# Optimization experiments

Hardware: AMD Instinct MI355X
Metric: run time of the kernel (lower is better)

Reference implementation:

```python
import jax, jax.numpy as jnp
import numpy as np

B, T, IN, OUT, H = 1024, 25, 96, 96, 2048


def setup_inputs() -> dict:
    key = jax.random.key(0)
    ks = jax.random.split(key, 16)
    s = 0.05  # small init scale to keep gates in linear-ish region
    return {
        "input": jax.random.normal(ks[0], (B, IN), jnp.float32),
        "future_poses": jax.random.normal(ks[1], (B, T, OUT), jnp.float32),
        "hiddens": jax.random.normal(ks[2], (2, B, H), jnp.float32) * s,
        "W_ih0": jax.random.normal(ks[3], (3 * H, IN), jnp.float32) * s,
        "W_hh0": jax.random.normal(ks[4], (3 * H, H), jnp.float32) * s,
        "b_ih0": jax.random.normal(ks[5], (3 * H,), jnp.float32) * s,
        "b_hh0": jax.random.normal(ks[6], (3 * H,), jnp.float32) * s,
        "W_ih1": jax.random.normal(ks[7], (3 * H, H), jnp.float32) * s,
        "W_hh1": jax.random.normal(ks[8], (3 * H, H), jnp.float32) * s,
        "b_ih1": jax.random.normal(ks[9], (3 * H,), jnp.float32) * s,
        "b_hh1": jax.random.normal(ks[10], (3 * H,), jnp.float32) * s,
        "W_fc": jax.random.normal(ks[11], (OUT, H), jnp.float32) * s,
        "b_fc": jax.random.normal(ks[12], (OUT,), jnp.float32) * s,
        "teacher_forcing_rate": 0,
    }


def gru_cell(x, h, W_ih, W_hh, b_ih, b_hh):
    # PyTorch nn.GRUCell math; gate order [r, z, n]
    gi = x @ W_ih.T + b_ih
    gh = h @ W_hh.T + b_hh
    i_r, i_z, i_n = jnp.split(gi, 3, axis=-1)
    h_r, h_z, h_n = jnp.split(gh, 3, axis=-1)
    r = jax.nn.sigmoid(i_r + h_r)
    z = jax.nn.sigmoid(i_z + h_z)
    n = jnp.tanh(i_n + r * h_n)
    return (1.0 - z) * n + z * h


def reference(input, future_poses, hiddens, W_ih0, W_hh0, b_ih0, b_hh0,
              W_ih1, W_hh1, b_ih1, b_hh1, W_fc, b_fc, teacher_forcing_rate):
    # dropout p=0.0 (eval) -> identity; teacher_forcing_rate=0 -> always
    def step(carry, _):
        dec_in, h0, h1 = carry
        h0 = gru_cell(dec_in, h0, W_ih0, W_hh0, b_ih0, b_hh0)
        h1 = gru_cell(h0, h1, W_ih1, W_hh1, b_ih1, b_hh1)
        out = jax.nn.sigmoid(h1 @ W_fc.T + b_fc)  # [B, OUT]
        dec_in = jax.lax.stop_gradient(out)       # torch .detach()
        return (dec_in, h0, h1), out

    carry0 = (input, hiddens[0], hiddens[1])
    _, outs = jax.lax.scan(step, carry0, None, length=T)  # [T, B, OUT]
    return jnp.transpose(outs, (1, 0, 2))  # [B, T, OUT]
```

## Files before the change

kernel.cpp:

```cpp
#include <hip/hip_runtime.h>
#include <stdint.h>

typedef __bf16 bf16;
typedef __attribute__((ext_vector_type(8))) __bf16 bf16x8;
typedef __attribute__((ext_vector_type(4))) float f32x4;

#define GRU_H 2048
#define ODIM 96
#define PADX 128
#define BATCH 1024
#define TSTEPS 25

__device__ __forceinline__ float sigm(float x) { return 1.f / (1.f + __expf(-x)); }

__device__ __forceinline__ void gload16(const void* g, void* l) {
  __builtin_amdgcn_global_load_lds((const __attribute__((address_space(1))) uint32_t*)g,
                                   (__attribute__((address_space(3))) uint32_t*)l, 16, 0, 0);
}

__global__ void k_cvt(const float* __restrict__ s, bf16* __restrict__ d, int n) {
  int stride = gridDim.x * blockDim.x;
  for (int i = blockIdx.x * blockDim.x + threadIdx.x; i < n; i += stride)
    d[i] = (bf16)s[i];
}

__global__ void k_cvt_pad(const float* __restrict__ s, bf16* __restrict__ d,
                          int rows, int cin, int cout) {
  int n = rows * cout;
  int stride = gridDim.x * blockDim.x;
  for (int i = blockIdx.x * blockDim.x + threadIdx.x; i < n; i += stride) {
    int r = i / cout, c = i - r * cout;
    d[i] = (c < cin) ? (bf16)s[r * cin + c] : (bf16)0.f;
  }
}

__global__ void k_init_h(const float* __restrict__ s, float* __restrict__ hf,
                         bf16* __restrict__ hb, int n) {
  int stride = gridDim.x * blockDim.x;
  for (int i = blockIdx.x * blockDim.x + threadIdx.x; i < n; i += stride) {
    float v = s[i];
    hf[i] = v;
    hb[i] = (bf16)v;
  }
}

__global__ __launch_bounds__(512, 1) void k_gru(
    const bf16* __restrict__ xb, int kx,
    const bf16* __restrict__ hb,
    const bf16* __restrict__ wih,
    const bf16* __restrict__ whh,
    const float* __restrict__ bih, const float* __restrict__ bhh,
    const float* __restrict__ hprevf,
    float* __restrict__ hnewf, bf16* __restrict__ hnewb) {
  __shared__ alignas(16) char sm[3][40960];

  const int tid = threadIdx.x;
  const int l = tid & 63;
  const int w = tid >> 6;
  const int wm = w >> 1, wn = w & 1;
  const int bn0 = blockIdx.x * 64;
  const int bm0 = blockIdx.y * 128;
  const int lm = l >> 4, ln = l & 15;

  const int S1 = GRU_H / 64;
  const int S2 = kx / 64;
  const int S = S1 + S2;

  f32x4 accR[2][2] = {};
  f32x4 accZ[2][2] = {};
  f32x4 accNH[2][2] = {};
  f32x4 accNI[2][2] = {};

  auto stageStep = [&](int buf, int step) {
    const bf16* A; const bf16* W; int K; int k0;
    if (step < S1) { A = hb; W = whh; K = GRU_H; k0 = step * 64; }
    else           { A = xb; W = wih; K = kx;    k0 = (step - S1) * 64; }
    char* sb = &sm[buf][0];
#pragma unroll
    for (int it = 0; it < 2; ++it) {
      int c = it * 512 + tid;
      int row = c >> 3, pos = c & 7, slot = pos ^ (row & 7);
      const bf16* src = A + (size_t)(bm0 + row) * K + k0 + slot * 8;
      char* dst = sb + ((it * 512 + (tid & ~63)) << 4);
      gload16(src, dst);
    }
#pragma unroll
    for (int it = 0; it < 3; ++it) {
      int c = it * 512 + tid;
      int row = c >> 3, pos = c & 7, slot = pos ^ (row & 7);
      int g = row >> 6, r = row & 63;
      const bf16* src = W + (size_t)(g * GRU_H + bn0 + r) * K + k0 + slot * 8;
      char* dst = sb + 16384 + ((it * 512 + (tid & ~63)) << 4);
      gload16(src, dst);
    }
  };

  auto computeStep = [&](int buf, f32x4 (&accN)[2][2]) {
    const char* bp = &sm[buf][0];
#pragma unroll
    for (int kf = 0; kf < 2; ++kf) {
      bf16x8 af[2];
#pragma unroll
      for (int mf = 0; mf < 2; ++mf) {
        int row = wm * 32 + mf * 16 + ln;
        int pos = (kf * 4 + lm) ^ (row & 7);
        af[mf] = *(const bf16x8*)(bp + row * 128 + (pos << 4));
      }
      bf16x8 bq[3][2];
#pragma unroll
      for (int g = 0; g < 3; ++g)
#pragma unroll
        for (int nf = 0; nf < 2; ++nf) {
          int row = g * 64 + wn * 32 + nf * 16 + ln;
          int pos = (kf * 4 + lm) ^ (row & 7);
          bq[g][nf] = *(const bf16x8*)(bp + 16384 + row * 128 + (pos << 4));
        }
#pragma unroll
      for (int mf = 0; mf < 2; ++mf)
#pragma unroll
        for (int nf = 0; nf < 2; ++nf) {
          accR[mf][nf] = __builtin_amdgcn_mfma_f32_16x16x32_bf16(af[mf], bq[0][nf], accR[mf][nf], 0, 0, 0);
          accZ[mf][nf] = __builtin_amdgcn_mfma_f32_16x16x32_bf16(af[mf], bq[1][nf], accZ[mf][nf], 0, 0, 0);
          accN[mf][nf] = __builtin_amdgcn_mfma_f32_16x16x32_bf16(af[mf], bq[2][nf], accN[mf][nf], 0, 0, 0);
        }
    }
  };

  stageStep(0, 0);
  stageStep(1, 1);

  int bc = 0;
  for (int s = 0; s < S; ++s) {
    if (s + 2 < S) {
      int b2 = bc + 2; if (b2 >= 3) b2 -= 3;
      stageStep(b2, s + 2);
      asm volatile("s_waitcnt vmcnt(10)" ::: "memory");
    } else if (s + 1 < S) {
      asm volatile("s_waitcnt vmcnt(5)" ::: "memory");
    } else {
      asm volatile("s_waitcnt vmcnt(0)" ::: "memory");
    }
    __builtin_amdgcn_s_barrier();
    if (s < S1) computeStep(bc, accNH);
    else        computeStep(bc, accNI);
    asm volatile("s_waitcnt lgkmcnt(0)" ::: "memory");
    __builtin_amdgcn_s_barrier();
    ++bc; if (bc == 3) bc = 0;
  }

#pragma unroll
  for (int nf = 0; nf < 2; ++nf) {
    int j = bn0 + wn * 32 + nf * 16 + ln;
    float br = bih[j] + bhh[j];
    float bz = bih[GRU_H + j] + bhh[GRU_H + j];
    float bin = bih[2 * GRU_H + j];
    float bhn = bhh[2 * GRU_H + j];
#pragma unroll
    for (int mf = 0; mf < 2; ++mf) {
#pragma unroll
      for (int rr = 0; rr < 4; ++rr) {
        int m = bm0 + wm * 32 + mf * 16 + lm * 4 + rr;
        size_t idx = (size_t)m * GRU_H + j;
        float hp = hprevf[idx];
        float rg = sigm(accR[mf][nf][rr] + br);
        float zg = sigm(accZ[mf][nf][rr] + bz);
        float ng = tanhf(accNI[mf][nf][rr] + bin + rg * (accNH[mf][nf][rr] + bhn));
        float hn = (1.f - zg) * ng + zg * hp;
        hnewf[idx] = hn;
        hnewb[idx] = (bf16)hn;
      }
    }
  }
}

__global__ __launch_bounds__(256, 1) void k_fc_part(const bf16* __restrict__ h1b,
                                                    const bf16* __restrict__ wfc,
                                                    float* __restrict__ part) {
  const int kc = blockIdx.x;
  const int mt = blockIdx.y;
  const int l = threadIdx.x & 63, w = threadIdx.x >> 6;
  const int lm = l >> 4, ln = l & 15;
  const int m0 = mt * 64 + w * 16;
  const int k0 = kc * 128;
  f32x4 acc[6] = {};
#pragma unroll
  for (int kf = 0; kf < 4; ++kf) {
    bf16x8 a = *(const bf16x8*)&h1b[(size_t)(m0 + ln) * GRU_H + k0 + kf * 32 + lm * 8];
#pragma unroll
    for (int nf = 0; nf < 6; ++nf) {
      bf16x8 b = *(const bf16x8*)&wfc[(size_t)(nf * 16 + ln) * GRU_H + k0 + kf * 32 + lm * 8];
      acc[nf] = __builtin_amdgcn_mfma_f32_16x16x32_bf16(a, b, acc[nf], 0, 0, 0);
    }
  }
  float* base = part + (size_t)kc * (BATCH * ODIM);
#pragma unroll
  for (int nf = 0; nf < 6; ++nf)
#pragma unroll
    for (int rr = 0; rr < 4; ++rr)
      base[(size_t)(m0 + lm * 4 + rr) * ODIM + nf * 16 + ln] = acc[nf][rr];
}

__global__ void k_fc_red(const float* __restrict__ part, const float* __restrict__ bfc,
                         float* __restrict__ dout, bf16* __restrict__ decb, int t) {
  int i = blockIdx.x * blockDim.x + threadIdx.x;
  if (i >= BATCH * ODIM) return;
  int m = i / ODIM, n = i - m * ODIM;
  float s = bfc[n];
#pragma unroll
  for (int kc = 0; kc < 16; ++kc) s += part[(size_t)kc * (BATCH * ODIM) + i];
  s = sigm(s);
  dout[(size_t)m * (TSTEPS * ODIM) + t * ODIM + n] = s;
  decb[m * PADX + n] = (bf16)s;
}

extern "C" void kernel_launch(void* const* d_in, const int* in_sizes, int n_in,
                              void* d_out, int out_size, void* d_ws, size_t ws_size,
                              hipStream_t stream) {
  const float* input   = (const float*)d_in[0];
  const float* hiddens = (const float*)d_in[2];
  const float* W_ih0   = (const float*)d_in[3];
  const float* W_hh0   = (const float*)d_in[4];
  const float* b_ih0   = (const float*)d_in[5];
  const float* b_hh0   = (const float*)d_in[6];
  const float* W_ih1   = (const float*)d_in[7];
  const float* W_hh1   = (const float*)d_in[8];
  const float* b_ih1   = (const float*)d_in[9];
  const float* b_hh1   = (const float*)d_in[10];
  const float* W_fc    = (const float*)d_in[11];
  const float* b_fc    = (const float*)d_in[12];
  float* out = (float*)d_out;

  char* p = (char*)d_ws;
  auto take = [&](size_t n) { char* q = p; p += (n + 255) & ~(size_t)255; return q; };
  bf16* wih0b = (bf16*)take((size_t)3 * GRU_H * PADX * 2);
  bf16* whh0b = (bf16*)take((size_t)3 * GRU_H * GRU_H * 2);
  bf16* wih1b = (bf16*)take((size_t)3 * GRU_H * GRU_H * 2);
  bf16* whh1b = (bf16*)take((size_t)3 * GRU_H * GRU_H * 2);
  bf16* wfcb  = (bf16*)take((size_t)ODIM * GRU_H * 2);
  bf16* decb  = (bf16*)take((size_t)BATCH * PADX * 2);
  float* h0f[2], *h1f[2];
  bf16* h0b[2], *h1b[2];
  h0f[0] = (float*)take((size_t)BATCH * GRU_H * 4);
  h0f[1] = (float*)take((size_t)BATCH * GRU_H * 4);
  h1f[0] = (float*)take((size_t)BATCH * GRU_H * 4);
  h1f[1] = (float*)take((size_t)BATCH * GRU_H * 4);
  h0b[0] = (bf16*)take((size_t)BATCH * GRU_H * 2);
  h0b[1] = (bf16*)take((size_t)BATCH * GRU_H * 2);
  h1b[0] = (bf16*)take((size_t)BATCH * GRU_H * 2);
  h1b[1] = (bf16*)take((size_t)BATCH * GRU_H * 2);
  float* fcpart = (float*)take((size_t)16 * BATCH * ODIM * 4);

  k_cvt_pad<<<768, 256, 0, stream>>>(W_ih0, wih0b, 3 * GRU_H, ODIM, PADX);
  k_cvt<<<2048, 256, 0, stream>>>(W_hh0, whh0b, 3 * GRU_H * GRU_H);
  k_cvt<<<2048, 256, 0, stream>>>(W_ih1, wih1b, 3 * GRU_H * GRU_H);
  k_cvt<<<2048, 256, 0, stream>>>(W_hh1, whh1b, 3 * GRU_H * GRU_H);
  k_cvt<<<192, 256, 0, stream>>>(W_fc, wfcb, ODIM * GRU_H);
  k_cvt_pad<<<512, 256, 0, stream>>>(input, decb, BATCH, ODIM, PADX);
  k_init_h<<<2048, 256, 0, stream>>>(hiddens, h0f[0], h0b[0], BATCH * GRU_H);
  k_init_h<<<2048, 256, 0, stream>>>(hiddens + (size_t)BATCH * GRU_H, h1f[0], h1b[0], BATCH * GRU_H);

  int cur = 0;
  for (int t = 0; t < TSTEPS; ++t) {
    int nxt = cur ^ 1;
    k_gru<<<dim3(32, 8), 512, 0, stream>>>(decb, PADX, h0b[cur], wih0b, whh0b,
                                           b_ih0, b_hh0, h0f[cur], h0f[nxt], h0b[nxt]);
    k_gru<<<dim3(32, 8), 512, 0, stream>>>(h0b[nxt], GRU_H, h1b[cur], wih1b, whh1b,
                                           b_ih1, b_hh1, h1f[cur], h1f[nxt], h1b[nxt]);
    k_fc_part<<<dim3(16, 16), 256, 0, stream>>>(h1b[nxt], wfcb, fcpart);
    k_fc_red<<<384, 256, 0, stream>>>(fcpart, b_fc, out, decb, t);
    cur = nxt;
  }
}
```

Baseline: 2.830 ms.

## Shrink GRU GEMM tile to 64x64 with 256 threads and double buffering

The fused GRU gate GEMM kernel now uses 64-row M tiles with 4 waves of 256 threads, each wave owning a 16-column slice across all 64 rows, instead of 128-row tiles with 8 waves. The grid doubles to 512 blocks, and the 3-stage LDS ring with split barriers becomes a 2-buffer ping-pong using 64KB LDS. Dropping the launch-bound minimum of one block allows two or more blocks per CU, which should improve occupancy and latency hiding on 256 CUs. The cost is that each weight tile is reused across fewer batch rows, so weight traffic from L2 doubles. The pipeline is also shallower, with a full vmcnt(0) wait every step.

```diff
diff --git a/kernel.cpp b/kernel.cpp
--- a/kernel.cpp
+++ b/kernel.cpp
@@ -44,7 +44,7 @@
   }
 }
 
-__global__ __launch_bounds__(512, 1) void k_gru(
+__global__ __launch_bounds__(256) void k_gru(
     const bf16* __restrict__ xb, int kx,
     const bf16* __restrict__ hb,
     const bf16* __restrict__ wih,
@@ -52,119 +52,107 @@
     const float* __restrict__ bih, const float* __restrict__ bhh,
     const float* __restrict__ hprevf,
     float* __restrict__ hnewf, bf16* __restrict__ hnewb) {
-  __shared__ alignas(16) char sm[3][40960];
+  __shared__ alignas(16) char sm[2][32768];
 
   const int tid = threadIdx.x;
   const int l = tid & 63;
-  const int w = tid >> 6;
-  const int wm = w >> 1, wn = w & 1;
+  const int wn = tid >> 6;
+  const int wb = tid & ~63;
   const int bn0 = blockIdx.x * 64;
-  const int bm0 = blockIdx.y * 128;
+  const int bm0 = blockIdx.y * 64;
   const int lm = l >> 4, ln = l & 15;
+  char* sm0 = &sm[0][0];
 
   const int S1 = GRU_H / 64;
   const int S2 = kx / 64;
-  const int S = S1 + S2;
-
-  f32x4 accR[2][2] = {};
-  f32x4 accZ[2][2] = {};
-  f32x4 accNH[2][2] = {};
-  f32x4 accNI[2][2] = {};
-
-  auto stageStep = [&](int buf, int step) {
-    const bf16* A; const bf16* W; int K; int k0;
-    if (step < S1) { A = hb; W = whh; K = GRU_H; k0 = step * 64; }
-    else           { A = xb; W = wih; K = kx;    k0 = (step - S1) * 64; }
-    char* sb = &sm[buf][0];
+
+  f32x4 accR[4] = {};
+  f32x4 accZ[4] = {};
+  f32x4 accNH[4] = {};
+  f32x4 accNI[4] = {};
+
+  auto stage = [&](int lb2, const bf16* __restrict__ A, const bf16* __restrict__ W,
+                   int K, int k0) {
+    char* sb = sm0 + lb2;
 #pragma unroll
     for (int it = 0; it < 2; ++it) {
-      int c = it * 512 + tid;
+      int c = it * 256 + tid;
       int row = c >> 3, pos = c & 7, slot = pos ^ (row & 7);
-      const bf16* src = A + (size_t)(bm0 + row) * K + k0 + slot * 8;
-      char* dst = sb + ((it * 512 + (tid & ~63)) << 4);
-      gload16(src, dst);
-    }
-#pragma unroll
-    for (int it = 0; it < 3; ++it) {
-      int c = it * 512 + tid;
+      gload16(A + (size_t)(bm0 + row) * K + k0 + slot * 8,
+              sb + ((it * 256 + wb) << 4));
+    }
+#pragma unroll
+    for (int it = 0; it < 6; ++it) {
+      int c = it * 256 + tid;
       int row = c >> 3, pos = c & 7, slot = pos ^ (row & 7);
       int g = row >> 6, r = row & 63;
-      const bf16* src = W + (size_t)(g * GRU_H + bn0 + r) * K + k0 + slot * 8;
-      char* dst = sb + 16384 + ((it * 512 + (tid & ~63)) << 4);
-      gload16(src, dst);
+      gload16(W + (size_t)(g * GRU_H + bn0 + r) * K + k0 + slot * 8,
+              sb + 8192 + ((it * 256 + wb) << 4));
     }
   };
 
-  auto computeStep = [&](int buf, f32x4 (&accN)[2][2]) {
-    const char* bp = &sm[buf][0];
+  auto computeStep = [&](int lb2, f32x4 (&accN)[4]) {
+    const char* bp = sm0 + lb2;
 #pragma unroll
     for (int kf = 0; kf < 2; ++kf) {
-      bf16x8 af[2];
-#pragma unroll
-      for (int mf = 0; mf < 2; ++mf) {
-        int row = wm * 32 + mf * 16 + ln;
+      bf16x8 af[4];
+#pragma unroll
+      for (int mf = 0; mf < 4; ++mf) {
+        int row = mf * 16 + ln;
         int pos = (kf * 4 + lm) ^ (row & 7);
         af[mf] = *(const bf16x8*)(bp + row * 128 + (pos << 4));
       }
-      bf16x8 bq[3][2];
-#pragma unroll
-      for (int g = 0; g < 3; ++g)
-#pragma unroll
-        for (int nf = 0; nf < 2; ++nf) {
-          int row = g * 64 + wn * 32 + nf * 16 + ln;
-          int pos = (kf * 4 + lm) ^ (row & 7);
-          bq[g][nf] = *(const bf16x8*)(bp + 16384 + row * 128 + (pos << 4));
-        }
-#pragma unroll
-      for (int mf = 0; mf < 2; ++mf)
-#pragma unroll
-        for (int nf = 0; nf < 2; ++nf) {
-          accR[mf][nf] = __builtin_amdgcn_mfma_f32_16x16x32_bf16(af[mf], bq[0][nf], accR[mf][nf], 0, 0, 0);
-          accZ[mf][nf] = __builtin_amdgcn_mfma_f32_16x16x32_bf16(af[mf], bq[1][nf], accZ[mf][nf], 0, 0, 0);
-          accN[mf][nf] = __builtin_amdgcn_mfma_f32_16x16x32_bf16(af[mf], bq[2][nf], accN[mf][nf], 0, 0, 0);
-        }
+#pragma unroll
+      for (int g = 0; g < 3; ++g) {
+        int row = g * 64 + wn * 16 + ln;
+        int pos = (kf * 4 + lm) ^ (row & 7);
+        bf16x8 bq = *(const bf16x8*)(bp + 8192 + row * 128 + (pos << 4));
+        f32x4* accG = (g == 0) ? accR : (g == 1) ? accZ : accN;
+#pragma unroll
+        for (int mf = 0; mf < 4; ++mf)
+          accG[mf] = __builtin_amdgcn_mfma_f32_16x16x32_bf16(af[mf], bq, accG[mf], 0, 0, 0);
+      }
     }
   };
 
-  stageStep(0, 0);
-  stageStep(1, 1);
-
-  int bc = 0;
-  for (int s = 0; s < S; ++s) {
-    if (s + 2 < S) {
-      int b2 = bc + 2; if (b2 >= 3) b2 -= 3;
-      stageStep(b2, s + 2);
-      asm volatile("s_waitcnt vmcnt(10)" ::: "memory");
-    } else if (s + 1 < S) {
-      asm volatile("s_waitcnt vmcnt(5)" ::: "memory");
+  stage(0, hb, whh, GRU_H, 0);
+  asm volatile("s_waitcnt vmcnt(0)\ns_barrier" ::: "memory");
+
+  int lb = 0;
+  for (int s = 0; s < S1; ++s) {
+    if (s + 1 < S1) stage(lb ^ 32768, hb, whh, GRU_H, (s + 1) * 64);
+    else            stage(lb ^ 32768, xb, wih, kx, 0);
+    computeStep(lb, accNH);
+    asm volatile("s_waitcnt vmcnt(0) lgkmcnt(0)\ns_barrier" ::: "memory");
+    lb ^= 32768;
+  }
+  for (int s = 0; s < S2; ++s) {
+    if (s + 1 < S2) {
+      stage(lb ^ 32768, xb, wih, kx, (s + 1) * 64);
+      computeStep(lb, accNI);
+      asm volatile("s_waitcnt vmcnt(0) lgkmcnt(0)\ns_barrier" ::: "memory");
+      lb ^= 32768;
     } else {
-      asm volatile("s_waitcnt vmcnt(0)" ::: "memory");
-    }
-    __builtin_amdgcn_s_barrier();
-    if (s < S1) computeStep(bc, accNH);
-    else        computeStep(bc, accNI);
-    asm volatile("s_waitcnt lgkmcnt(0)" ::: "memory");
-    __builtin_amdgcn_s_barrier();
-    ++bc; if (bc == 3) bc = 0;
-  }
-
-#pragma unroll
-  for (int nf = 0; nf < 2; ++nf) {
-    int j = bn0 + wn * 32 + nf * 16 + ln;
+      computeStep(lb, accNI);
+    }
+  }
+
+  {
+    int j = bn0 + wn * 16 + ln;
     float br = bih[j] + bhh[j];
     float bz = bih[GRU_H + j] + bhh[GRU_H + j];
     float bin = bih[2 * GRU_H + j];
     float bhn = bhh[2 * GRU_H + j];
 #pragma unroll
-    for (int mf = 0; mf < 2; ++mf) {
+    for (int mf = 0; mf < 4; ++mf) {
 #pragma unroll
       for (int rr = 0; rr < 4; ++rr) {
-        int m = bm0 + wm * 32 + mf * 16 + lm * 4 + rr;
+        int m = bm0 + mf * 16 + lm * 4 + rr;
         size_t idx = (size_t)m * GRU_H + j;
         float hp = hprevf[idx];
-        float rg = sigm(accR[mf][nf][rr] + br);
-        float zg = sigm(accZ[mf][nf][rr] + bz);
-        float ng = tanhf(accNI[mf][nf][rr] + bin + rg * (accNH[mf][nf][rr] + bhn));
+        float rg = sigm(accR[mf][rr] + br);
+        float zg = sigm(accZ[mf][rr] + bz);
+        float ng = tanhf(accNI[mf][rr] + bin + rg * (accNH[mf][rr] + bhn));
         float hn = (1.f - zg) * ng + zg * hp;
         hnewf[idx] = hn;
         hnewb[idx] = (bf16)hn;
@@ -262,10 +250,10 @@
   int cur = 0;
   for (int t = 0; t < TSTEPS; ++t) {
     int nxt = cur ^ 1;
-    k_gru<<<dim3(32, 8), 512, 0, stream>>>(decb, PADX, h0b[cur], wih0b, whh0b,
-                                           b_ih0, b_hh0, h0f[cur], h0f[nxt], h0b[nxt]);
-    k_gru<<<dim3(32, 8), 512, 0, stream>>>(h0b[nxt], GRU_H, h1b[cur], wih1b, whh1b,
-                                           b_ih1, b_hh1, h1f[cur], h1f[nxt], h1b[nxt]);
+    k_gru<<<dim3(32, 16), 256, 0, stream>>>(decb, PADX, h0b[cur], wih0b, whh0b,
+                                            b_ih0, b_hh0, h0f[cur], h0f[nxt], h0b[nxt]);
+    k_gru<<<dim3(32, 16), 256, 0, stream>>>(h0b[nxt], GRU_H, h1b[cur], wih1b, whh1b,
+                                            b_ih1, b_hh1, h1f[cur], h1f[nxt], h1b[nxt]);
     k_fc_part<<<dim3(16, 16), 256, 0, stream>>>(h1b[nxt], wfcb, fcpart);
     k_fc_red<<<384, 256, 0, stream>>>(fcpart, b_fc, out, decb, t);
     cur = nxt;
```

Result: no change. 2.874 ms (+1.5%).
